# Optimization experiments

Hardware: AMD Instinct MI355X
Metric: run time of the kernel (lower is better)

Reference implementation:

```python
import jax, jax.numpy as jnp
import numpy as np

K_HOPS = 10  # truncation order of the heat-kernel Taylor series


def setup_inputs() -> dict:
    key = jax.random.key(0)
    k1, k2, k3 = jax.random.split(key, 3)
    N, E, D_IN, D_OUT = 50000, 625000, 128, 128
    x = jax.random.normal(k1, (N, D_IN), dtype=jnp.float32)
    edge_index = jax.random.randint(k2, (2, E), 0, N, dtype=jnp.int64)
    t = jnp.asarray(5.0, dtype=jnp.float32)  # learnable diffusion time
    lim = 1.0 / np.sqrt(D_IN)
    W = jax.random.uniform(k3, (D_OUT, D_IN), dtype=jnp.float32, minval=-lim, maxval=lim)
    b = jnp.zeros((D_OUT,), dtype=jnp.float32)
    return {"x": x, "edge_index": edge_index, "t": t, "W": W, "b": b}


def reference(x, edge_index, t, W, b):
    N = x.shape[0]
    loop = jnp.arange(N, dtype=edge_index.dtype)
    src = jnp.concatenate([edge_index[0], loop])  # gcn_norm adds self-loops
    dst = jnp.concatenate([edge_index[1], loop])
    # symmetric normalization: norm_e = deg(dst)^-1/2 * deg(src)^-1/2
    deg = jnp.zeros((N,), dtype=x.dtype).at[dst].add(1.0)
    dinv = jnp.where(deg > 0, jax.lax.rsqrt(deg), 0.0)
    norm = dinv[src] * dinv[dst]  # [E+N]

    def prop(h):  # one hop of A_hat @ h via gather-scale-scatter
        msg = h[src] * norm[:, None]          # [E+N, D]
        return jax.ops.segment_sum(msg, dst, num_segments=N)

    # heat kernel: e^{-t} * sum_k t^k/k! * A_hat^k x
    coeff = jnp.exp(-t)
    out = coeff * x
    h = x
    for k in range(1, K_HOPS + 1):
        h = prop(h)
        coeff = coeff * t / k
        out = out + coeff * h
    return out @ W.T + b
```

## Files before the change

### kernel.cpp

```cpp
#include <hip/hip_runtime.h>
#include <math.h>

typedef float f4 __attribute__((ext_vector_type(4)));
typedef float f8 __attribute__((ext_vector_type(8)));
typedef _Float16 h8 __attribute__((ext_vector_type(8)));


__global__ void k_count(const int* __restrict__ dst, int* __restrict__ cnt, int E) {
  int e = blockIdx.x * blockDim.x + threadIdx.x;
  if (e < E) atomicAdd(&cnt[dst[e]], 1);
}

__global__ void k_scan_partial(const int* __restrict__ cnt, int* __restrict__ rowptr,
                               int* __restrict__ bsums, float* __restrict__ dinv, int N) {
  __shared__ int s[1024];
  int tid = threadIdx.x;
  int idx = blockIdx.x * 1024 + tid;
  int v = (idx < N) ? cnt[idx] : 0;
  if (idx < N) dinv[idx] = rsqrtf((float)(v + 1));
  s[tid] = v;
  __syncthreads();
  for (int off = 1; off < 1024; off <<= 1) {
    int add = (tid >= off) ? s[tid - off] : 0;
    __syncthreads();
    s[tid] += add;
    __syncthreads();
  }
  if (idx <= N) rowptr[idx] = s[tid] - v;
  if (tid == 1023) bsums[blockIdx.x] = s[1023];
}

__global__ void k_scan_sums(int* __restrict__ bsums, int nb) {
  __shared__ int s[1024];
  int tid = threadIdx.x;
  int v = (tid < nb) ? bsums[tid] : 0;
  s[tid] = v;
  __syncthreads();
  for (int off = 1; off < 1024; off <<= 1) {
    int add = (tid >= off) ? s[tid - off] : 0;
    __syncthreads();
    s[tid] += add;
    __syncthreads();
  }
  if (tid < nb) bsums[tid] = s[tid] - v;
}

__global__ void k_add_offsets(int* __restrict__ rowptr, int* __restrict__ cursor,
                              const int* __restrict__ bsums, int N) {
  int idx = blockIdx.x * 1024 + threadIdx.x;
  if (idx <= N) {
    int v = rowptr[idx] + bsums[blockIdx.x];
    rowptr[idx] = v;
    if (idx < N) cursor[idx] = v;
  }
}

__global__ void k_scatter(const int* __restrict__ src, const int* __restrict__ dst,
                          const float* __restrict__ dinv, int* __restrict__ cursor,
                          int2* __restrict__ colw, int E) {
  int e = blockIdx.x * blockDim.x + threadIdx.x;
  if (e < E) {
    int s = src[e];
    int d = dst[e];
    int slot = atomicAdd(&cursor[d], 1);
    colw[slot] = make_int2(s, __float_as_int(dinv[s] * dinv[d]));
  }
}

__global__ void k_tohalf(const float* __restrict__ x, _Float16* __restrict__ xh, int total8) {
  int i = blockIdx.x * blockDim.x + threadIdx.x;
  if (i < total8) {
    f4 a = ((const f4*)x)[i * 2], b = ((const f4*)x)[i * 2 + 1];
    f8 v = {a.x, a.y, a.z, a.w, b.x, b.y, b.z, b.w};
    ((h8*)xh)[i] = __builtin_convertvector(v, h8);
  }
}

__global__ __launch_bounds__(256) void k_hop(
    const int* __restrict__ rowptr, const int2* __restrict__ colw,
    const float* __restrict__ dinv, const h8* __restrict__ xh,
    const h8* __restrict__ yin, h8* __restrict__ yout,
    const float* __restrict__ t_ptr, int j, int first, int N) {
  int wave = threadIdx.x >> 6;
  int lane = threadIdx.x & 63;
  int quarter = lane >> 4;
  int fl = lane & 15;
  int r = (blockIdx.x * 4 + wave) * 4 + quarter;
  if (r >= N) return;
  float t = t_ptr[0];
  float cj = expf(-t);
  for (int i = 1; i <= j; ++i) cj *= t / (float)i;
  float gs = first ? cj * t / (float)(j + 1) : 1.0f;

  auto G = [&](int idx) -> f8 {
    return __builtin_convertvector(yin[(size_t)idx * 16 + fl], f8);
  };

  f8 sA = {0,0,0,0,0,0,0,0}, sB = sA, sC = sA, sD = sA;
  int e = rowptr[r], end = rowptr[r + 1];
  for (; e + 3 < end; e += 4) {
    int2 c0 = colw[e], c1 = colw[e + 1], c2 = colw[e + 2], c3 = colw[e + 3];
    sA += __int_as_float(c0.y) * G(c0.x);
    sB += __int_as_float(c1.y) * G(c1.x);
    sC += __int_as_float(c2.y) * G(c2.x);
    sD += __int_as_float(c3.y) * G(c3.x);
  }
  for (; e < end; ++e) {
    int2 c0 = colw[e];
    sA += __int_as_float(c0.y) * G(c0.x);
  }
  f8 s = (sA + sB) + (sC + sD);
  float di = dinv[r];
  s += (di * di) * G(r);
  f8 xr = __builtin_convertvector(xh[(size_t)r * 16 + fl], f8);
  s = gs * s + cj * xr;
  yout[(size_t)r * 16 + fl] = __builtin_convertvector(s, h8);
}

__global__ __launch_bounds__(256) void k_matmul(
    const h8* __restrict__ y16, const float* __restrict__ W,
    const float* __restrict__ bias, float* __restrict__ out, int N) {
  __shared__ h8 whiS[128 * 16];
  __shared__ h8 wloS[128 * 16];
  int tid = threadIdx.x;
  int rblk = blockIdx.x * 128;

#pragma unroll
  for (int it = 0; it < 8; ++it) {
    int idx = it * 256 + tid;
    int n = idx >> 4, g = idx & 15;
    f4 a = *(const f4*)&W[(size_t)n * 128 + g * 8];
    f4 b = *(const f4*)&W[(size_t)n * 128 + g * 8 + 4];
    f8 w = {a.x, a.y, a.z, a.w, b.x, b.y, b.z, b.w};
    h8 hi = __builtin_convertvector(w, h8);
    f8 hir = __builtin_convertvector(hi, f8);
    h8 lo = __builtin_convertvector(w - hir, h8);
    int slot = n * 16 + (g ^ (n & 7));
    whiS[slot] = hi;
    wloS[slot] = lo;
  }
  __syncthreads();

  int wave = tid >> 6, lane = tid & 63;
  int q = lane >> 4, fl = lane & 15;
  int rbase = rblk + wave * 32;

  f4 acc[2][8];
#pragma unroll
  for (int rt = 0; rt < 2; ++rt)
#pragma unroll
    for (int nt = 0; nt < 8; ++nt) acc[rt][nt] = (f4){0.f, 0.f, 0.f, 0.f};

#pragma unroll
  for (int s = 0; s < 4; ++s) {
    h8 aA, aB;
    {
      int r0 = rbase + fl;       if (r0 >= N) r0 = N - 1;
      int r1 = rbase + 16 + fl;  if (r1 >= N) r1 = N - 1;
      aA = y16[(size_t)r0 * 16 + s * 4 + q];
      aB = y16[(size_t)r1 * 16 + s * 4 + q];
    }
#pragma unroll
    for (int nt = 0; nt < 8; ++nt) {
      int n = nt * 16 + fl;
      int slot = n * 16 + ((s * 4 + q) ^ (n & 7));
      h8 bh = whiS[slot];
      h8 bl = wloS[slot];
      acc[0][nt] = __builtin_amdgcn_mfma_f32_16x16x32_f16(aA, bh, acc[0][nt], 0, 0, 0);
      acc[0][nt] = __builtin_amdgcn_mfma_f32_16x16x32_f16(aA, bl, acc[0][nt], 0, 0, 0);
      acc[1][nt] = __builtin_amdgcn_mfma_f32_16x16x32_f16(aB, bh, acc[1][nt], 0, 0, 0);
      acc[1][nt] = __builtin_amdgcn_mfma_f32_16x16x32_f16(aB, bl, acc[1][nt], 0, 0, 0);
    }
  }

#pragma unroll
  for (int rt = 0; rt < 2; ++rt) {
#pragma unroll
    for (int nt = 0; nt < 8; ++nt) {
      float bv = bias[nt * 16 + fl];
#pragma unroll
      for (int reg = 0; reg < 4; ++reg) {
        int r = rbase + rt * 16 + q * 4 + reg;
        if (r < N) out[(size_t)r * 128 + nt * 16 + fl] = acc[rt][nt][reg] + bv;
      }
    }
  }
}


extern "C" void kernel_launch(void* const* d_in, const int* in_sizes, int n_in,
                              void* d_out, int out_size, void* d_ws, size_t ws_size,
                              hipStream_t stream) {
  const float* x = (const float*)d_in[0];
  const int* ei = (const int*)d_in[1];
  const float* t = (const float*)d_in[2];
  const float* W = (const float*)d_in[3];
  const float* b = (const float*)d_in[4];
  int N = in_sizes[0] / 128;
  int E = in_sizes[1] / 2;
  const int* srcp = ei;
  const int* dstp = ei + E;
  float* out = (float*)d_out;

  char* ws = (char*)d_ws;
  size_t off = 0;
  auto alloc = [&](size_t bytes) -> void* {
    void* p = ws + off;
    off += (bytes + 255) & ~(size_t)255;
    return p;
  };
  h8*    yh0    = (h8*)alloc((size_t)N * 128 * 2);
  h8*    yh1    = (h8*)alloc((size_t)N * 128 * 2);
  h8*    xh     = (h8*)alloc((size_t)N * 128 * 2);
  int*   cnt    = (int*)alloc((size_t)N * 4);
  float* dinv   = (float*)alloc((size_t)N * 4);
  int*   rowptr = (int*)alloc((size_t)(N + 1) * 4);
  int*   cursor = (int*)alloc((size_t)N * 4);
  int*   bsums  = (int*)alloc(4096);
  int2*  colw   = (int2*)alloc((size_t)E * 8);
  (void)ws_size;

  int nb_scan = (N + 1 + 1023) / 1024;

  hipMemsetAsync(cnt, 0, (size_t)N * 4, stream);
  k_count<<<(E + 255) / 256, 256, 0, stream>>>(dstp, cnt, E);
  k_scan_partial<<<nb_scan, 1024, 0, stream>>>(cnt, rowptr, bsums, dinv, N);
  k_scan_sums<<<1, 1024, 0, stream>>>(bsums, nb_scan);
  k_add_offsets<<<nb_scan, 1024, 0, stream>>>(rowptr, cursor, bsums, N);
  k_scatter<<<(E + 255) / 256, 256, 0, stream>>>(srcp, dstp, dinv, cursor, colw, E);
  k_tohalf<<<(N * 16 + 255) / 256, 256, 0, stream>>>(x, (_Float16*)xh, N * 16);

  int nblk = (N + 15) / 16;
  const h8* yin = xh;
  h8* bufs[2] = {yh0, yh1};
  for (int m = 0; m < 10; ++m) {
    h8* yout = bufs[m & 1];
    k_hop<<<nblk, 256, 0, stream>>>(rowptr, colw, dinv, xh, yin, yout,
                                    t, 9 - m, (m == 0) ? 1 : 0, N);
    yin = yout;
  }

  k_matmul<<<(N + 127) / 128, 256, 0, stream>>>(yin, W, b, out, N);
}
```

Before: 458.0 us.

## Pad CSR rows to multiples of four and load edges as int4 pairs

Rounds each row's edge count up to a multiple of four in the scan. The padded slots are zero-filled by a memset of the whole edge array, so they contribute weight 0 from node 0. This lets the hop kernel drop its scalar tail loop and fetch two edges per 16-byte int4 load. It also remaps lanes so each row's 16 feature lanes are split into two groups of eight. The cost is extra padded edges per hop (about 1.5 per row on average), a larger memset, and gathers of node 0 for padding entries.

```diff
diff --git a/kernel.cpp b/kernel.cpp
--- a/kernel.cpp
+++ b/kernel.cpp
@@ -18,7 +18,8 @@
   int idx = blockIdx.x * 1024 + tid;
   int v = (idx < N) ? cnt[idx] : 0;
   if (idx < N) dinv[idx] = rsqrtf((float)(v + 1));
-  s[tid] = v;
+  int vp = (v + 3) & ~3;
+  s[tid] = vp;
   __syncthreads();
   for (int off = 1; off < 1024; off <<= 1) {
     int add = (tid >= off) ? s[tid - off] : 0;
@@ -26,7 +27,7 @@
     s[tid] += add;
     __syncthreads();
   }
-  if (idx <= N) rowptr[idx] = s[tid] - v;
+  if (idx <= N) rowptr[idx] = s[tid] - vp;
   if (tid == 1023) bsums[blockIdx.x] = s[1023];
 }
 
@@ -83,10 +84,10 @@
     const float* __restrict__ t_ptr, int j, int first, int N) {
   int wave = threadIdx.x >> 6;
   int lane = threadIdx.x & 63;
-  int quarter = lane >> 4;
-  int fl = lane & 15;
-  int r = (blockIdx.x * 4 + wave) * 4 + quarter;
+  int grp = lane >> 3;
+  int r = (blockIdx.x * 4 + wave) * 4 + (grp >> 1);
   if (r >= N) return;
+  int fl = (lane & 7) + (grp & 1) * 8;
   float t = t_ptr[0];
   float cj = expf(-t);
   for (int i = 1; i <= j; ++i) cj *= t / (float)i;
@@ -98,16 +99,13 @@
 
   f8 sA = {0,0,0,0,0,0,0,0}, sB = sA, sC = sA, sD = sA;
   int e = rowptr[r], end = rowptr[r + 1];
-  for (; e + 3 < end; e += 4) {
-    int2 c0 = colw[e], c1 = colw[e + 1], c2 = colw[e + 2], c3 = colw[e + 3];
-    sA += __int_as_float(c0.y) * G(c0.x);
-    sB += __int_as_float(c1.y) * G(c1.x);
-    sC += __int_as_float(c2.y) * G(c2.x);
-    sD += __int_as_float(c3.y) * G(c3.x);
-  }
-  for (; e < end; ++e) {
-    int2 c0 = colw[e];
-    sA += __int_as_float(c0.y) * G(c0.x);
+  for (; e < end; e += 4) {
+    int4 p0 = *(const int4*)&colw[e];
+    int4 p1 = *(const int4*)&colw[e + 2];
+    sA += __int_as_float(p0.y) * G(p0.x);
+    sB += __int_as_float(p0.w) * G(p0.z);
+    sC += __int_as_float(p1.y) * G(p1.x);
+    sD += __int_as_float(p1.w) * G(p1.z);
   }
   f8 s = (sA + sB) + (sC + sD);
   float di = dinv[r];
@@ -217,12 +215,14 @@
   int*   rowptr = (int*)alloc((size_t)(N + 1) * 4);
   int*   cursor = (int*)alloc((size_t)N * 4);
   int*   bsums  = (int*)alloc(4096);
-  int2*  colw   = (int2*)alloc((size_t)E * 8);
+  size_t colw_bytes = ((size_t)E + 4 * (size_t)N) * 8;
+  int2*  colw   = (int2*)alloc(colw_bytes);
   (void)ws_size;
 
   int nb_scan = (N + 1 + 1023) / 1024;
 
   hipMemsetAsync(cnt, 0, (size_t)N * 4, stream);
+  hipMemsetAsync(colw, 0, colw_bytes, stream);
   k_count<<<(E + 255) / 256, 256, 0, stream>>>(dstp, cnt, E);
   k_scan_partial<<<nb_scan, 1024, 0, stream>>>(cnt, rowptr, bsums, dinv, N);
   k_scan_sums<<<1, 1024, 0, stream>>>(bsums, nb_scan);
```

Measured after the change: 445.2 us. -2.8%, faster.
